# Performance work log

Hardware: AMD Instinct MI355X
Metric: run time of the kernel (lower is better)

The kernel has to match this reference:

```python
import jax, jax.numpy as jnp
import numpy as np

N, E, B = 50000, 800000, 256
NODE_DIM, EDGE_DIM, H = 4, 1, 64


def setup_inputs() -> dict:
    key = jax.random.key(0)
    ks = jax.random.split(key, 32)
    def rn(k, shape, scale=0.1):
        return (jax.random.normal(k, shape) * scale).astype(jnp.float32)
    inp = {
        "x": jax.random.normal(ks[0], (N, NODE_DIM), dtype=jnp.float32),
        "edge_index": jax.random.randint(ks[1], (2, E), 0, N, dtype=jnp.int32),
        "edge_attr": jax.random.normal(ks[2], (E, EDGE_DIM), dtype=jnp.float32),
        "batch": jnp.sort(jax.random.randint(ks[3], (N,), 0, B, dtype=jnp.int32)),
        # embed Linear(node_dim -> H); weights stored [in, out]
        "embed_W": rn(ks[4], (NODE_DIM, H)), "embed_b": jnp.zeros((H,), jnp.float32),
        # GATv2 conv1
        "c1_Wl": rn(ks[5], (H, H)), "c1_bl": jnp.zeros((H,), jnp.float32),
        "c1_Wr": rn(ks[6], (H, H)), "c1_br": jnp.zeros((H,), jnp.float32),
        "c1_We": rn(ks[7], (EDGE_DIM, H)),
        "c1_att": rn(ks[8], (H,)), "c1_bias": jnp.zeros((H,), jnp.float32),
        # GATv2 conv2
        "c2_Wl": rn(ks[9], (H, H)), "c2_bl": jnp.zeros((H,), jnp.float32),
        "c2_Wr": rn(ks[10], (H, H)), "c2_br": jnp.zeros((H,), jnp.float32),
        "c2_We": rn(ks[11], (EDGE_DIM, H)),
        "c2_att": rn(ks[12], (H,)), "c2_bias": jnp.zeros((H,), jnp.float32),
        # ODE func: Linear(H, 2H) -> tanh -> Linear(2H, H)
        "ode_W1": rn(ks[13], (H, 2 * H)), "ode_b1": jnp.zeros((2 * H,), jnp.float32),
        "ode_W2": rn(ks[14], (2 * H, H)), "ode_b2": jnp.zeros((H,), jnp.float32),
        # predictor: Linear(2H, 32) -> SiLU -> (Dropout eval=id) -> Linear(32, 1)
        "pred_W1": rn(ks[15], (2 * H, 32)), "pred_b1": jnp.zeros((32,), jnp.float32),
        "pred_W2": rn(ks[16], (32, 1)), "pred_b2": jnp.zeros((1,), jnp.float32),
    }
    return inp


def gatv2_conv(x, src, dst, edge_attr, Wl, bl, Wr, br, We, att, bias):
    # PyG GATv2Conv, heads=1: xl feeds messages (source), xr the target side.
    xl = x @ Wl + bl                       # [N,H]
    xr = x @ Wr + br                       # [N,H]
    m = xl[src] + xr[dst] + edge_attr @ We  # [E,H]
    m = jnp.where(m > 0, m, 0.2 * m)        # leaky_relu(0.2)
    e = m @ att                             # [E]
    emax = jax.ops.segment_max(e, dst, num_segments=N)
    ex = jnp.exp(e - emax[dst])
    denom = jax.ops.segment_sum(ex, dst, num_segments=N)
    alpha = ex / denom[dst]                 # softmax over incoming edges
    out = jax.ops.segment_sum(alpha[:, None] * xl[src], dst, num_segments=N)
    return out + bias


def reference(x, edge_index, edge_attr, batch,
              embed_W, embed_b,
              c1_Wl, c1_bl, c1_Wr, c1_br, c1_We, c1_att, c1_bias,
              c2_Wl, c2_bl, c2_Wr, c2_br, c2_We, c2_att, c2_bias,
              ode_W1, ode_b1, ode_W2, ode_b2,
              pred_W1, pred_b1, pred_W2, pred_b2):
    src, dst = edge_index[0], edge_index[1]
    silu = jax.nn.silu
    h = x @ embed_W + embed_b
    h = silu(gatv2_conv(h, src, dst, edge_attr, c1_Wl, c1_bl, c1_Wr, c1_br, c1_We, c1_att, c1_bias))
    h = silu(gatv2_conv(h, src, dst, edge_attr, c2_Wl, c2_bl, c2_Wr, c2_br, c2_We, c2_att, c2_bias))

    # one fixed-grid RK4 step from t=0 to t=1 (torchdiffeq rk4 on t=[0,1])
    def f(y):
        return jnp.tanh(y @ ode_W1 + ode_b1) @ ode_W2 + ode_b2
    k1 = f(h)
    k2 = f(h + 0.5 * k1)
    k3 = f(h + 0.5 * k2)
    k4 = f(h + k3)
    h = h + (k1 + 2.0 * k2 + 2.0 * k3 + k4) / 6.0

    # global mean / max pool over graphs
    counts = jax.ops.segment_sum(jnp.ones((N,), h.dtype), batch, num_segments=B)
    gmean = jax.ops.segment_sum(h, batch, num_segments=B) / jnp.maximum(counts, 1.0)[:, None]
    gmax = jax.ops.segment_max(h, batch, num_segments=B)
    gmax = jnp.where(counts[:, None] > 0, gmax, 0.0)
    g = jnp.concatenate([gmean, gmax], axis=1)  # [B, 2H]

    out = silu(g @ pred_W1 + pred_b1) @ pred_W2 + pred_b2  # dropout in eval = identity
    return out[:, 0]
```

## Files before the change

### kernel.cpp

```cpp
#include <hip/hip_runtime.h>
#include <math.h>

#define Nn 50000
#define Ee 800000
#define Bb 256
#define Hh 64
#define TPB 256
#define CHUNK 512

__device__ __forceinline__ float tanh_fast(float x) {
    return 1.f - 2.f / (__expf(2.f * x) + 1.f);
}

__global__ void k_embed(const float* __restrict__ x, const float* __restrict__ W,
                        const float* __restrict__ b, float* __restrict__ h) {
    int idx = blockIdx.x * blockDim.x + threadIdx.x;
    if (idx >= Nn * Hh) return;
    int n = idx >> 6, j = idx & 63;
    float acc = b[j];
#pragma unroll
    for (int d = 0; d < 4; ++d) acc += x[n * 4 + d] * W[d * Hh + j];
    h[idx] = acc;
}

__global__ void k_hist(const int* __restrict__ dst, int* __restrict__ counts) {
    int e = blockIdx.x * blockDim.x + threadIdx.x;
    if (e < Ee) atomicAdd(&counts[dst[e]], 1);
}

__global__ void k_scan1(const int* __restrict__ counts, int* __restrict__ off,
                        int* __restrict__ chunksum) {
    __shared__ int s[CHUNK];
    int t = threadIdx.x;
    int base = blockIdx.x * CHUNK;
    int v = (base + t < Nn) ? counts[base + t] : 0;
    s[t] = v;
    __syncthreads();
    for (int d = 1; d < CHUNK; d <<= 1) {
        int u = (t >= d) ? s[t - d] : 0;
        __syncthreads();
        s[t] += u;
        __syncthreads();
    }
    if (base + t < Nn) off[base + t + 1] = s[t];
    if (t == CHUNK - 1) chunksum[blockIdx.x] = s[t];
}

__global__ void k_scan2(int* __restrict__ chunksum, int nch) {
    if (blockIdx.x == 0 && threadIdx.x == 0) {
        int run = 0;
        for (int i = 0; i < nch; ++i) { int v = chunksum[i]; chunksum[i] = run; run += v; }
    }
}

__global__ void k_scan3(int* __restrict__ off, const int* __restrict__ chunkoff,
                        int* __restrict__ cursor) {
    int i = blockIdx.x * blockDim.x + threadIdx.x;
    if (i > Nn) return;
    int v;
    if (i == 0) { off[0] = 0; v = 0; }
    else {
        v = off[i] + chunkoff[(i - 1) >> 9];
        off[i] = v;
    }
    if (i < Nn) cursor[i] = v;
}

__global__ void k_scatter(const int* __restrict__ src, const int* __restrict__ dst,
                          const float* __restrict__ ea, int* __restrict__ cursor,
                          int2* __restrict__ epack) {
    int e = blockIdx.x * blockDim.x + threadIdx.x;
    if (e >= Ee) return;
    int d = dst[e];
    int p = atomicAdd(&cursor[d], 1);
    epack[p] = make_int2(src[e], __float_as_int(ea[e]));
}

__global__ __launch_bounds__(256) void k_lin(const float* __restrict__ h,
                      const float* __restrict__ Wl, const float* __restrict__ bl,
                      const float* __restrict__ Wr, const float* __restrict__ br,
                      float* __restrict__ xl, float* __restrict__ xr) {
    int lane = threadIdx.x & 63, w = threadIdx.x >> 6;
    int n0 = blockIdx.x * 16 + w * 4;
    float al[4], ar[4];
#pragma unroll
    for (int q = 0; q < 4; ++q) { al[q] = bl[lane]; ar[q] = br[lane]; }
    for (int i4 = 0; i4 < 16; ++i4) {
        float4 hv[4];
#pragma unroll
        for (int q = 0; q < 4; ++q)
            hv[q] = *(const float4*)(h + (n0 + q) * 64 + i4 * 4);
#pragma unroll
        for (int u = 0; u < 4; ++u) {
            int i = i4 * 4 + u;
            float wlv = Wl[i * 64 + lane];
            float wrv = Wr[i * 64 + lane];
#pragma unroll
            for (int q = 0; q < 4; ++q) {
                float hq = ((const float*)&hv[q])[u];
                al[q] += hq * wlv;
                ar[q] += hq * wrv;
            }
        }
    }
#pragma unroll
    for (int q = 0; q < 4; ++q) {
        xl[(n0 + q) * 64 + lane] = al[q];
        xr[(n0 + q) * 64 + lane] = ar[q];
    }
}

__global__ void k_conv(const float* __restrict__ xl, const float* __restrict__ xr,
                       const int2* __restrict__ epack, const int* __restrict__ off,
                       const float* __restrict__ We, const float* __restrict__ att,
                       const float* __restrict__ bias, float* __restrict__ hout) {
    int gid = blockIdx.x * blockDim.x + threadIdx.x;
    int n = gid >> 6, lane = gid & 63;
    if (n >= Nn) return;
    int g = lane >> 4, l16 = lane & 15;
    int s = off[n], t = off[n + 1];
    float4 xr4 = *(const float4*)(xr + (size_t)n * 64 + l16 * 4);
    float4 We4 = *(const float4*)(We + l16 * 4);
    float4 at4 = *(const float4*)(att + l16 * 4);
    float4 acc = make_float4(0.f, 0.f, 0.f, 0.f);
    float m_run = -1e30f, s_run = 0.f;
    for (int c = s; c < t; c += 4) {
        int e = c + g;
        bool valid = e < t;
        int2 pk = valid ? epack[e] : epack[c];
        int sr = pk.x;
        float ceav = valid ? __int_as_float(pk.y) : 0.f;
        float4 row = *(const float4*)(xl + (size_t)sr * 64 + l16 * 4);
        float mx_ = row.x + xr4.x + ceav * We4.x;
        float my_ = row.y + xr4.y + ceav * We4.y;
        float mz_ = row.z + xr4.z + ceav * We4.z;
        float mw_ = row.w + xr4.w + ceav * We4.w;
        mx_ = mx_ > 0.f ? mx_ : 0.2f * mx_;
        my_ = my_ > 0.f ? my_ : 0.2f * my_;
        mz_ = mz_ > 0.f ? mz_ : 0.2f * mz_;
        mw_ = mw_ > 0.f ? mw_ : 0.2f * mw_;
        float pv = mx_ * at4.x + my_ * at4.y + mz_ * at4.z + mw_ * at4.w;
#pragma unroll
        for (int o = 1; o < 16; o <<= 1) pv += __shfl_xor(pv, o);
        float ee = valid ? pv : -1e30f;
        float cm = ee;
        cm = fmaxf(cm, __shfl_xor(cm, 16));
        cm = fmaxf(cm, __shfl_xor(cm, 32));
        float m_new = fmaxf(m_run, cm);
        float f = __expf(m_run - m_new);
        acc.x *= f; acc.y *= f; acc.z *= f; acc.w *= f; s_run *= f;
        float w = __expf(ee - m_new);
        acc.x += w * row.x; acc.y += w * row.y;
        acc.z += w * row.z; acc.w += w * row.w;
        s_run += w;
        m_run = m_new;
    }
#pragma unroll
    for (int o = 16; o <= 32; o <<= 1) {
        acc.x += __shfl_xor(acc.x, o); acc.y += __shfl_xor(acc.y, o);
        acc.z += __shfl_xor(acc.z, o); acc.w += __shfl_xor(acc.w, o);
        s_run += __shfl_xor(s_run, o);
    }
    float4 b4 = *(const float4*)(bias + l16 * 4);
    float inv = (t > s) ? 1.f / s_run : 0.f;
    float4 o4;
    o4.x = acc.x * inv + b4.x; o4.y = acc.y * inv + b4.y;
    o4.z = acc.z * inv + b4.z; o4.w = acc.w * inv + b4.w;
    o4.x = o4.x / (1.f + __expf(-o4.x));
    o4.y = o4.y / (1.f + __expf(-o4.y));
    o4.z = o4.z / (1.f + __expf(-o4.z));
    o4.w = o4.w / (1.f + __expf(-o4.w));
    if (lane < 16) *(float4*)(hout + (size_t)n * 64 + l16 * 4) = o4;
}

__global__ __launch_bounds__(256) void k_ode4(float* __restrict__ h,
        const float* __restrict__ W1, const float* __restrict__ b1,
        const float* __restrict__ W2, const float* __restrict__ b2) {
    __shared__ float yt[16][64];
    __shared__ float zt[16][128];
    int t = threadIdx.x;
    int nb = blockIdx.x * 16;
    int j = t & 63, wg = t >> 6;
    int k = t & 127, kg = t >> 7;
    {
        int nn = t >> 4, jj = (t & 15) * 4;
        *(float4*)&yt[nn][jj] = *(const float4*)(h + (size_t)(nb + nn) * 64 + jj);
    }
    float h0[4], ksum[4];
#pragma unroll
    for (int q = 0; q < 4; ++q) {
        h0[q] = h[(size_t)(nb + wg * 4 + q) * 64 + j];
        ksum[q] = 0.f;
    }
    __syncthreads();
#pragma unroll
    for (int s = 0; s < 4; ++s) {
        const float wgt = (s == 1 || s == 2) ? 2.f : 1.f;
        const float cf = (s == 2) ? 1.f : 0.5f;
        {
            float acc1[8];
#pragma unroll
            for (int q = 0; q < 8; ++q) acc1[q] = b1[k];
            for (int i4 = 0; i4 < 16; ++i4) {
                float wv4[4];
#pragma unroll
                for (int u = 0; u < 4; ++u) wv4[u] = W1[(i4 * 4 + u) * 128 + k];
                float4 yv[8];
#pragma unroll
                for (int q8 = 0; q8 < 8; ++q8)
                    yv[q8] = *(const float4*)&yt[kg * 8 + q8][i4 * 4];
#pragma unroll
                for (int u = 0; u < 4; ++u)
#pragma unroll
                    for (int q8 = 0; q8 < 8; ++q8)
                        acc1[q8] += ((const float*)&yv[q8])[u] * wv4[u];
            }
#pragma unroll
            for (int q = 0; q < 8; ++q) zt[kg * 8 + q][k] = tanh_fast(acc1[q]);
        }
        __syncthreads();
        {
            float acc2[4];
#pragma unroll
            for (int q = 0; q < 4; ++q) acc2[q] = b2[j];
            for (int k4 = 0; k4 < 32; ++k4) {
                float wv2[4];
#pragma unroll
                for (int u = 0; u < 4; ++u) wv2[u] = W2[(k4 * 4 + u) * 64 + j];
                float4 zv[4];
#pragma unroll
                for (int q = 0; q < 4; ++q)
                    zv[q] = *(const float4*)&zt[wg * 4 + q][k4 * 4];
#pragma unroll
                for (int u = 0; u < 4; ++u)
#pragma unroll
                    for (int q = 0; q < 4; ++q)
                        acc2[q] += ((const float*)&zv[q])[u] * wv2[u];
            }
#pragma unroll
            for (int q = 0; q < 4; ++q) {
                ksum[q] += wgt * acc2[q];
                if (s < 3) yt[wg * 4 + q][j] = h0[q] + cf * acc2[q];
            }
        }
        __syncthreads();
    }
#pragma unroll
    for (int q = 0; q < 4; ++q)
        h[(size_t)(nb + wg * 4 + q) * 64 + j] = h0[q] + ksum[q] * (1.f / 6.f);
}

__global__ void k_binit(int* __restrict__ gs, int* __restrict__ ge) {
    int b = threadIdx.x;
    if (b < Bb) { gs[b] = 0; ge[b] = 0; }
}

__global__ void k_bounds(const int* __restrict__ batch, int* __restrict__ gs,
                         int* __restrict__ ge) {
    int n = blockIdx.x * blockDim.x + threadIdx.x;
    if (n >= Nn) return;
    int b = batch[n];
    if (n == 0 || batch[n - 1] != b) gs[b] = n;
    if (n == Nn - 1 || batch[n + 1] != b) ge[b] = n + 1;
}

__global__ void k_pool(const float* __restrict__ h, const int* __restrict__ gs,
                       const int* __restrict__ ge, float* __restrict__ g) {
    int b = blockIdx.x;
    int s = gs[b], e = ge[b];
    int w = threadIdx.x >> 6, lane = threadIdx.x & 63;
    float sum = 0.f, mx = -1e30f;
    for (int n = s + w; n < e; n += 4) {
        float v = h[n * Hh + lane];
        sum += v;
        mx = fmaxf(mx, v);
    }
    __shared__ float ssum[4][64], smx[4][64];
    ssum[w][lane] = sum;
    smx[w][lane] = mx;
    __syncthreads();
    if (threadIdx.x < 64) {
        int j = threadIdx.x;
        float su = ssum[0][j] + ssum[1][j] + ssum[2][j] + ssum[3][j];
        float m2 = fmaxf(fmaxf(smx[0][j], smx[1][j]), fmaxf(smx[2][j], smx[3][j]));
        int cnt = e - s;
        g[b * 2 * Hh + j] = (cnt > 0) ? su / (float)cnt : 0.f;
        g[b * 2 * Hh + Hh + j] = (cnt > 0) ? m2 : 0.f;
    }
}

__global__ void k_pred(const float* __restrict__ g, const float* __restrict__ W1,
                       const float* __restrict__ b1, const float* __restrict__ W2,
                       const float* __restrict__ b2, float* __restrict__ out) {
    int gid = blockIdx.x * blockDim.x + threadIdx.x;
    int b = gid >> 6, lane = gid & 63;
    if (b >= Bb) return;
    int hh = lane & 31, half = lane >> 5;
    const float* gr = g + b * 2 * Hh + half * Hh;
    float a = 0.f;
#pragma unroll 8
    for (int i = 0; i < Hh; ++i) a += gr[i] * W1[(half * Hh + i) * 32 + hh];
    a += __shfl_xor(a, 32);
    a += b1[hh];
    float sl = a / (1.f + expf(-a));
    float partial = (half == 0) ? sl * W2[hh] : 0.f;
#pragma unroll
    for (int o = 32; o > 0; o >>= 1) partial += __shfl_xor(partial, o);
    if (lane == 0) out[b] = partial + b2[0];
}

extern "C" void kernel_launch(void* const* d_in, const int* in_sizes, int n_in,
                              void* d_out, int out_size, void* d_ws, size_t ws_size,
                              hipStream_t stream) {
    const float* x     = (const float*)d_in[0];
    const int*   ei    = (const int*)d_in[1];
    const float* ea    = (const float*)d_in[2];
    const int*   batch = (const int*)d_in[3];
    const float* embW  = (const float*)d_in[4];
    const float* embB  = (const float*)d_in[5];
    const float* c1Wl = (const float*)d_in[6];  const float* c1bl = (const float*)d_in[7];
    const float* c1Wr = (const float*)d_in[8];  const float* c1br = (const float*)d_in[9];
    const float* c1We = (const float*)d_in[10]; const float* c1att = (const float*)d_in[11];
    const float* c1bias = (const float*)d_in[12];
    const float* c2Wl = (const float*)d_in[13]; const float* c2bl = (const float*)d_in[14];
    const float* c2Wr = (const float*)d_in[15]; const float* c2br = (const float*)d_in[16];
    const float* c2We = (const float*)d_in[17]; const float* c2att = (const float*)d_in[18];
    const float* c2bias = (const float*)d_in[19];
    const float* oW1 = (const float*)d_in[20]; const float* ob1 = (const float*)d_in[21];
    const float* oW2 = (const float*)d_in[22]; const float* ob2 = (const float*)d_in[23];
    const float* pW1 = (const float*)d_in[24]; const float* pb1 = (const float*)d_in[25];
    const float* pW2 = (const float*)d_in[26]; const float* pb2 = (const float*)d_in[27];
    float* out = (float*)d_out;

    float* fws = (float*)d_ws;
    size_t NH = (size_t)Nn * Hh;
    float* h    = fws;
    float* xl   = fws + NH;
    float* xr   = fws + 2 * NH;
    int2*  epack = (int2*)(fws + 3 * NH);
    float* g    = (float*)(epack + Ee);
    int* iws = (int*)(g + (size_t)Bb * 128);
    int* counts = iws;
    int* off    = counts + Nn;
    int* cursor = off + Nn + 1;
    int* chk    = cursor + Nn;
    int* gs     = chk + 128;
    int* ge     = gs + Bb;

    const int* src = ei;
    const int* dst = ei + Ee;

    hipMemsetAsync(counts, 0, Nn * sizeof(int), stream);
    k_embed<<<(Nn * Hh + TPB - 1) / TPB, TPB, 0, stream>>>(x, embW, embB, h);
    k_hist<<<(Ee + TPB - 1) / TPB, TPB, 0, stream>>>(dst, counts);
    k_scan1<<<(Nn + CHUNK - 1) / CHUNK, CHUNK, 0, stream>>>(counts, off, chk);
    k_scan2<<<1, 64, 0, stream>>>(chk, (Nn + CHUNK - 1) / CHUNK);
    k_scan3<<<(Nn + 1 + TPB - 1) / TPB, TPB, 0, stream>>>(off, chk, cursor);
    k_scatter<<<(Ee + TPB - 1) / TPB, TPB, 0, stream>>>(src, dst, ea, cursor, epack);

    k_lin<<<Nn / 16, TPB, 0, stream>>>(h, c1Wl, c1bl, c1Wr, c1br, xl, xr);
    k_conv<<<(Nn * 64 + TPB - 1) / TPB, TPB, 0, stream>>>(xl, xr, epack, off, c1We, c1att, c1bias, h);

    k_lin<<<Nn / 16, TPB, 0, stream>>>(h, c2Wl, c2bl, c2Wr, c2br, xl, xr);
    k_conv<<<(Nn * 64 + TPB - 1) / TPB, TPB, 0, stream>>>(xl, xr, epack, off, c2We, c2att, c2bias, h);

    k_ode4<<<Nn / 16, 256, 0, stream>>>(h, oW1, ob1, oW2, ob2);

    k_binit<<<1, Bb, 0, stream>>>(gs, ge);
    k_bounds<<<(Nn + TPB - 1) / TPB, TPB, 0, stream>>>(batch, gs, ge);
    k_pool<<<Bb, 256, 0, stream>>>(h, gs, ge, g);
    k_pred<<<(Bb * 64 + TPB - 1) / TPB, TPB, 0, stream>>>(g, pW1, pb1, pW2, pb2, out);
}
```

Measured before the change: 604.3 us.

## Double per-thread register tile in RK4 kernel and fuse pooling with predictor

The ODE RK4 kernel now runs with 128 threads per block. Each thread computes two adjacent output columns for its row group and uses float2 loads of the weights, which halves weight-load instructions per FMA and raises register-level reuse of the shared-memory activations. Separately, the pooling and predictor kernels are merged so the pooled graph vector stays in shared memory, removing one launch and a global round-trip. The wider register tile raises register pressure, and there are fewer threads per block.

Result: slower. 845.5 us (+39.9%).

```diff
diff --git a/kernel.cpp b/kernel.cpp
--- a/kernel.cpp
+++ b/kernel.cpp
@@ -173,24 +173,27 @@
     if (lane < 16) *(float4*)(hout + (size_t)n * 64 + l16 * 4) = o4;
 }
 
-__global__ __launch_bounds__(256) void k_ode4(float* __restrict__ h,
+__global__ __launch_bounds__(128, 4) void k_ode4(float* __restrict__ h,
         const float* __restrict__ W1, const float* __restrict__ b1,
         const float* __restrict__ W2, const float* __restrict__ b2) {
     __shared__ float yt[16][64];
     __shared__ float zt[16][128];
     int t = threadIdx.x;
     int nb = blockIdx.x * 16;
-    int j = t & 63, wg = t >> 6;
-    int k = t & 127, kg = t >> 7;
-    {
-        int nn = t >> 4, jj = (t & 15) * 4;
-        *(float4*)&yt[nn][jj] = *(const float4*)(h + (size_t)(nb + nn) * 64 + jj);
-    }
-    float h0[4], ksum[4];
+    int kk = (t & 63) * 2, nh = t >> 6;
+    int jj = (t & 31) * 2, wg = t >> 5;
+#pragma unroll
+    for (int r = 0; r < 2; ++r) {
+        int f = t + r * 128;
+        int nn = f >> 4, c4 = (f & 15) * 4;
+        *(float4*)&yt[nn][c4] = *(const float4*)(h + (size_t)(nb + nn) * 64 + c4);
+    }
+    float h0[4][2], ksum[4][2];
 #pragma unroll
     for (int q = 0; q < 4; ++q) {
-        h0[q] = h[(size_t)(nb + wg * 4 + q) * 64 + j];
-        ksum[q] = 0.f;
+        float2 hv = *(const float2*)(h + (size_t)(nb + wg * 4 + q) * 64 + jj);
+        h0[q][0] = hv.x; h0[q][1] = hv.y;
+        ksum[q][0] = 0.f; ksum[q][1] = 0.f;
     }
     __syncthreads();
 #pragma unroll
@@ -198,35 +201,44 @@
         const float wgt = (s == 1 || s == 2) ? 2.f : 1.f;
         const float cf = (s == 2) ? 1.f : 0.5f;
         {
-            float acc1[8];
-#pragma unroll
-            for (int q = 0; q < 8; ++q) acc1[q] = b1[k];
+            float acc[8][2];
+            float2 bb = *(const float2*)(b1 + kk);
+#pragma unroll
+            for (int q = 0; q < 8; ++q) { acc[q][0] = bb.x; acc[q][1] = bb.y; }
             for (int i4 = 0; i4 < 16; ++i4) {
-                float wv4[4];
-#pragma unroll
-                for (int u = 0; u < 4; ++u) wv4[u] = W1[(i4 * 4 + u) * 128 + k];
+                float2 wv[4];
+#pragma unroll
+                for (int u = 0; u < 4; ++u)
+                    wv[u] = *(const float2*)(W1 + (size_t)(i4 * 4 + u) * 128 + kk);
                 float4 yv[8];
 #pragma unroll
-                for (int q8 = 0; q8 < 8; ++q8)
-                    yv[q8] = *(const float4*)&yt[kg * 8 + q8][i4 * 4];
+                for (int q = 0; q < 8; ++q)
+                    yv[q] = *(const float4*)&yt[nh * 8 + q][i4 * 4];
 #pragma unroll
                 for (int u = 0; u < 4; ++u)
 #pragma unroll
-                    for (int q8 = 0; q8 < 8; ++q8)
-                        acc1[q8] += ((const float*)&yv[q8])[u] * wv4[u];
+                    for (int q = 0; q < 8; ++q) {
+                        float yq = ((const float*)&yv[q])[u];
+                        acc[q][0] += yq * wv[u].x;
+                        acc[q][1] += yq * wv[u].y;
+                    }
             }
 #pragma unroll
-            for (int q = 0; q < 8; ++q) zt[kg * 8 + q][k] = tanh_fast(acc1[q]);
+            for (int q = 0; q < 8; ++q)
+                *(float2*)&zt[nh * 8 + q][kk] =
+                    make_float2(tanh_fast(acc[q][0]), tanh_fast(acc[q][1]));
         }
         __syncthreads();
         {
-            float acc2[4];
-#pragma unroll
-            for (int q = 0; q < 4; ++q) acc2[q] = b2[j];
+            float acc[4][2];
+            float2 bb = *(const float2*)(b2 + jj);
+#pragma unroll
+            for (int q = 0; q < 4; ++q) { acc[q][0] = bb.x; acc[q][1] = bb.y; }
             for (int k4 = 0; k4 < 32; ++k4) {
-                float wv2[4];
-#pragma unroll
-                for (int u = 0; u < 4; ++u) wv2[u] = W2[(k4 * 4 + u) * 64 + j];
+                float2 wv[4];
+#pragma unroll
+                for (int u = 0; u < 4; ++u)
+                    wv[u] = *(const float2*)(W2 + (size_t)(k4 * 4 + u) * 64 + jj);
                 float4 zv[4];
 #pragma unroll
                 for (int q = 0; q < 4; ++q)
@@ -234,20 +246,28 @@
 #pragma unroll
                 for (int u = 0; u < 4; ++u)
 #pragma unroll
-                    for (int q = 0; q < 4; ++q)
-                        acc2[q] += ((const float*)&zv[q])[u] * wv2[u];
+                    for (int q = 0; q < 4; ++q) {
+                        float zq = ((const float*)&zv[q])[u];
+                        acc[q][0] += zq * wv[u].x;
+                        acc[q][1] += zq * wv[u].y;
+                    }
             }
 #pragma unroll
             for (int q = 0; q < 4; ++q) {
-                ksum[q] += wgt * acc2[q];
-                if (s < 3) yt[wg * 4 + q][j] = h0[q] + cf * acc2[q];
+                ksum[q][0] += wgt * acc[q][0];
+                ksum[q][1] += wgt * acc[q][1];
+                if (s < 3)
+                    *(float2*)&yt[wg * 4 + q][jj] =
+                        make_float2(h0[q][0] + cf * acc[q][0], h0[q][1] + cf * acc[q][1]);
             }
         }
         __syncthreads();
     }
 #pragma unroll
     for (int q = 0; q < 4; ++q)
-        h[(size_t)(nb + wg * 4 + q) * 64 + j] = h0[q] + ksum[q] * (1.f / 6.f);
+        *(float2*)(h + (size_t)(nb + wg * 4 + q) * 64 + jj) =
+            make_float2(h0[q][0] + ksum[q][0] * (1.f / 6.f),
+                        h0[q][1] + ksum[q][1] * (1.f / 6.f));
 }
 
 __global__ void k_binit(int* __restrict__ gs, int* __restrict__ ge) {
@@ -264,8 +284,10 @@
     if (n == Nn - 1 || batch[n + 1] != b) ge[b] = n + 1;
 }
 
-__global__ void k_pool(const float* __restrict__ h, const int* __restrict__ gs,
-                       const int* __restrict__ ge, float* __restrict__ g) {
+__global__ void k_poolpred(const float* __restrict__ h, const int* __restrict__ gs,
+                           const int* __restrict__ ge, const float* __restrict__ W1,
+                           const float* __restrict__ b1, const float* __restrict__ W2,
+                           const float* __restrict__ b2, float* __restrict__ out) {
     int b = blockIdx.x;
     int s = gs[b], e = ge[b];
     int w = threadIdx.x >> 6, lane = threadIdx.x & 63;
@@ -276,6 +298,7 @@
         mx = fmaxf(mx, v);
     }
     __shared__ float ssum[4][64], smx[4][64];
+    __shared__ float gg[128];
     ssum[w][lane] = sum;
     smx[w][lane] = mx;
     __syncthreads();
@@ -284,29 +307,24 @@
         float su = ssum[0][j] + ssum[1][j] + ssum[2][j] + ssum[3][j];
         float m2 = fmaxf(fmaxf(smx[0][j], smx[1][j]), fmaxf(smx[2][j], smx[3][j]));
         int cnt = e - s;
-        g[b * 2 * Hh + j] = (cnt > 0) ? su / (float)cnt : 0.f;
-        g[b * 2 * Hh + Hh + j] = (cnt > 0) ? m2 : 0.f;
-    }
-}
-
-__global__ void k_pred(const float* __restrict__ g, const float* __restrict__ W1,
-                       const float* __restrict__ b1, const float* __restrict__ W2,
-                       const float* __restrict__ b2, float* __restrict__ out) {
-    int gid = blockIdx.x * blockDim.x + threadIdx.x;
-    int b = gid >> 6, lane = gid & 63;
-    if (b >= Bb) return;
-    int hh = lane & 31, half = lane >> 5;
-    const float* gr = g + b * 2 * Hh + half * Hh;
-    float a = 0.f;
+        gg[j] = (cnt > 0) ? su / (float)cnt : 0.f;
+        gg[64 + j] = (cnt > 0) ? m2 : 0.f;
+    }
+    __syncthreads();
+    if (threadIdx.x < 64) {
+        int hh = lane & 31, half = lane >> 5;
+        const float* gr = gg + half * 64;
+        float a = 0.f;
 #pragma unroll 8
-    for (int i = 0; i < Hh; ++i) a += gr[i] * W1[(half * Hh + i) * 32 + hh];
-    a += __shfl_xor(a, 32);
-    a += b1[hh];
-    float sl = a / (1.f + expf(-a));
-    float partial = (half == 0) ? sl * W2[hh] : 0.f;
-#pragma unroll
-    for (int o = 32; o > 0; o >>= 1) partial += __shfl_xor(partial, o);
-    if (lane == 0) out[b] = partial + b2[0];
+        for (int i = 0; i < Hh; ++i) a += gr[i] * W1[(half * Hh + i) * 32 + hh];
+        a += __shfl_xor(a, 32);
+        a += b1[hh];
+        float sl = a / (1.f + __expf(-a));
+        float partial = (half == 0) ? sl * W2[hh] : 0.f;
+#pragma unroll
+        for (int o = 32; o > 0; o >>= 1) partial += __shfl_xor(partial, o);
+        if (lane == 0) out[b] = partial + b2[0];
+    }
 }
 
 extern "C" void kernel_launch(void* const* d_in, const int* in_sizes, int n_in,
@@ -338,8 +356,7 @@
     float* xl   = fws + NH;
     float* xr   = fws + 2 * NH;
     int2*  epack = (int2*)(fws + 3 * NH);
-    float* g    = (float*)(epack + Ee);
-    int* iws = (int*)(g + (size_t)Bb * 128);
+    int* iws = (int*)(epack + Ee);
     int* counts = iws;
     int* off    = counts + Nn;
     int* cursor = off + Nn + 1;
@@ -364,10 +381,9 @@
     k_lin<<<Nn / 16, TPB, 0, stream>>>(h, c2Wl, c2bl, c2Wr, c2br, xl, xr);
     k_conv<<<(Nn * 64 + TPB - 1) / TPB, TPB, 0, stream>>>(xl, xr, epack, off, c2We, c2att, c2bias, h);
 
-    k_ode4<<<Nn / 16, 256, 0, stream>>>(h, oW1, ob1, oW2, ob2);
+    k_ode4<<<Nn / 16, 128, 0, stream>>>(h, oW1, ob1, oW2, ob2);
 
     k_binit<<<1, Bb, 0, stream>>>(gs, ge);
     k_bounds<<<(Nn + TPB - 1) / TPB, TPB, 0, stream>>>(batch, gs, ge);
-    k_pool<<<Bb, 256, 0, stream>>>(h, gs, ge, g);
-    k_pred<<<(Bb * 64 + TPB - 1) / TPB, TPB, 0, stream>>>(g, pW1, pb1, pW2, pb2, out);
-}
+    k_poolpred<<<Bb, 256, 0, stream>>>(h, gs, ge, pW1, pb1, pW2, pb2, out);
+}
```
